# Kernel optimization log

Hardware: AMD Instinct MI355X
Metric: run time of the kernel (lower is better)

## Reference

```python
import jax, jax.numpy as jnp
import numpy as np

NUM_EXPERTS = 256
TOP_K = 8
N_GROUP = 8
TOPK_GROUP = 4
ROUTED_SCALING = 2.5
EXPERTS_PER_GROUP = NUM_EXPERTS // N_GROUP  # 32


def setup_inputs() -> dict:
    key = jax.random.key(0)
    k1, k2, k3 = jax.random.split(key, 3)
    hidden_states = jax.random.normal(k1, (8192, 7168), dtype=jnp.float32)
    weight = jax.random.normal(k2, (NUM_EXPERTS, 7168), dtype=jnp.float32) * 0.02
    e_score_correction_bias = jax.random.normal(k3, (NUM_EXPERTS,), dtype=jnp.float32) * 0.1
    return {
        "hidden_states": hidden_states,
        "weight": weight,
        "e_score_correction_bias": e_score_correction_bias,
    }


def reference(hidden_states, weight, e_score_correction_bias):
    # Router logits: [T, E]
    router_logits = jnp.einsum("th,eh->te", hidden_states, weight)
    scores = jax.nn.sigmoid(router_logits)
    scores_for_choice = scores + e_score_correction_bias  # [T, E]

    T = scores_for_choice.shape[0]
    # Group-limited selection (noaux_tc): group score = sum of top-2 experts in group
    grouped = scores_for_choice.reshape(T, N_GROUP, EXPERTS_PER_GROUP)
    group_top2, _ = jax.lax.top_k(grouped, 2)            # [T, G, 2]
    group_scores = group_top2.sum(axis=-1)               # [T, G]
    _, group_idx = jax.lax.top_k(group_scores, TOPK_GROUP)  # [T, topk_group]
    group_mask = jax.nn.one_hot(group_idx, N_GROUP, dtype=scores.dtype).max(axis=1)  # [T, G]
    expert_mask = jnp.repeat(group_mask, EXPERTS_PER_GROUP, axis=-1)  # [T, E]
    masked_scores = scores_for_choice * expert_mask

    # Final top-k experts; routing weights gathered from raw sigmoid scores
    _, selected_experts = jax.lax.top_k(masked_scores, TOP_K)         # [T, K] int32
    routing_weights = jnp.take_along_axis(scores, selected_experts, axis=-1)  # [T, K]
    routing_weights = routing_weights / (routing_weights.sum(axis=-1, keepdims=True) + 1e-20)
    routing_weights = routing_weights * ROUTED_SCALING
    return routing_weights, selected_experts
```

## Files before the change

### kernel.cpp

```cpp
#include <hip/hip_runtime.h>
#include <math.h>
#include <stdint.h>

#define T_TOK 8192
#define NEXP  256
#define HD    7168
#define PLANE ((size_t)T_TOK * NEXP)
#define SCALE 4096.0f
#define INV_S2 (1.0f / 16777216.0f)
#define BM 64
#define BK 32
#define NSTEP_TOT (HD / BK)
#define BIMG_STEP 32768

typedef _Float16 h8  __attribute__((ext_vector_type(8)));
typedef float f32x16 __attribute__((ext_vector_type(16)));
typedef __attribute__((address_space(3))) uint8_t       lds_t;
typedef __attribute__((address_space(1))) const uint8_t gbl_t;

__global__ __launch_bounds__(256) void wconv(const float* __restrict__ W,
                                             _Float16* __restrict__ img) {
  const int cc  = blockIdx.x * 256 + threadIdx.x;
  const int t   = cc >> 11;
  const int c   = cc & 2047;
  const int hl  = c >> 10;
  const int rem = c & 1023;
  const int row = rem >> 2;
  const int sp  = rem & 3;
  const int sl  = sp ^ ((row >> 1) & 3);
  const int k   = t * BK + sl * 8;

  const float* src = W + (size_t)row * HD + k;
  const float4 v0 = *(const float4*)src;
  const float4 v1 = *(const float4*)(src + 4);
  const float xs[8] = {v0.x, v0.y, v0.z, v0.w, v1.x, v1.y, v1.z, v1.w};
  h8 out;
#pragma unroll
  for (int j = 0; j < 8; ++j) {
    const float v = xs[j] * SCALE;
    const _Float16 hh = (_Float16)v;
    out[j] = hl ? (_Float16)(v - (float)hh) : hh;
  }
  *(h8*)(img + (size_t)cc * 8) = out;
}

__global__ __launch_bounds__(256, 2) void router_gemm(
    const float* __restrict__ X, const _Float16* __restrict__ img,
    float* __restrict__ partial, int S) {
  __shared__ __align__(1024) _Float16 As[2][2][BM][BK];
  __shared__ __align__(1024) _Float16 Bs[2][2][NEXP][BK];

  const int tid = threadIdx.x;
  const int id  = blockIdx.x;
  const int sb  = id % S;
  const int mb  = id / S;

  const int row0  = mb * BM;
  const int nstep = (HD / S) / BK;
  const int tbase = sb * nstep;

  const int lane = tid & 63, wv = tid >> 6;
  const int r31 = lane & 31, kg = lane >> 5;

  const int sm = tid >> 2;
  const int sk = tid & 3;
  const int spA = sk ^ ((sm >> 1) & 3);

  const float* Ap = X + (size_t)(row0 + sm) * HD + tbase * BK + sk * 8;
  const uint8_t* imgB = (const uint8_t*)img + (size_t)tbase * BIMG_STEP + tid * 16;

  f32x16 accP[2][2], accQ[2][2];
#pragma unroll
  for (int i = 0; i < 2; ++i)
#pragma unroll
    for (int j = 0; j < 2; ++j) { accP[i][j] = (f32x16)(0.f); accQ[i][j] = (f32x16)(0.f); }

#define STAGE_B(t, b)                                                          \
  {                                                                            \
    const uint8_t* g = imgB + (size_t)(t) * BIMG_STEP;                         \
    uint8_t* l = (uint8_t*)&Bs[b][0][0][0] + tid * 16;                         \
    _Pragma("unroll")                                                          \
    for (int i = 0; i < 8; ++i)                                                \
      __builtin_amdgcn_global_load_lds((gbl_t*)(uintptr_t)(g + i * 4096),      \
                                       (lds_t*)(uintptr_t)(l + i * 4096),      \
                                       16, 0, 0);                              \
  }

#define CVT_WRITE_A(b, va, vb)                                                 \
  {                                                                            \
    const float xs[8] = {va.x, va.y, va.z, va.w, vb.x, vb.y, vb.z, vb.w};      \
    h8 hv, lv_;                                                                \
    _Pragma("unroll")                                                          \
    for (int j = 0; j < 8; ++j) {                                              \
      const float v = xs[j] * SCALE;                                           \
      const _Float16 hh = (_Float16)v;                                         \
      hv[j] = hh; lv_[j] = (_Float16)(v - (float)hh);                          \
    }                                                                          \
    *(h8*)&As[b][0][sm][spA * 8] = hv;                                         \
    *(h8*)&As[b][1][sm][spA * 8] = lv_;                                        \
  }

  {
    const float4 a0 = *(const float4*)(Ap);
    const float4 a1 = *(const float4*)(Ap + 4);
    __builtin_amdgcn_sched_barrier(0);
    STAGE_B(0, 0);
    asm volatile("s_waitcnt vmcnt(0)" ::: "memory");
    __builtin_amdgcn_sched_barrier(0);
    CVT_WRITE_A(0, a0, a1);
    asm volatile("s_waitcnt lgkmcnt(0)" ::: "memory");
    __builtin_amdgcn_s_barrier();
  }

  for (int t = 0; t < nstep; ++t) {
    const int cur = t & 1;
    const int nxt = cur ^ 1;
    const bool more = (t + 1 < nstep);

    float4 a0, a1;
    if (more) {
      const float* ap = Ap + (size_t)(t + 1) * BK;
      a0 = *(const float4*)(ap);
      a1 = *(const float4*)(ap + 4);
      __builtin_amdgcn_sched_barrier(0);
      STAGE_B(t + 1, nxt);
      __builtin_amdgcn_sched_barrier(0);
    }

    h8 aH[2][2], aL[2][2], bH[2][2], bL[2][2];
#pragma unroll
    for (int ks = 0; ks < 2; ++ks) {
#pragma unroll
      for (int mi = 0; mi < 2; ++mi) {
        const int row = mi * 32 + r31;
        const int sp  = (ks * 2 + kg) ^ ((row >> 1) & 3);
        aH[ks][mi] = *(const h8*)&As[cur][0][row][sp * 8];
        aL[ks][mi] = *(const h8*)&As[cur][1][row][sp * 8];
      }
#pragma unroll
      for (int ni = 0; ni < 2; ++ni) {
        const int col = wv * 64 + ni * 32 + r31;
        const int sp  = (ks * 2 + kg) ^ ((col >> 1) & 3);
        bH[ks][ni] = *(const h8*)&Bs[cur][0][col][sp * 8];
        bL[ks][ni] = *(const h8*)&Bs[cur][1][col][sp * 8];
      }
      __builtin_amdgcn_sched_barrier(0);
    }

    asm volatile("s_waitcnt lgkmcnt(8)" ::: "memory");
    __builtin_amdgcn_sched_barrier(0);
    __builtin_amdgcn_s_setprio(1);
#pragma unroll
    for (int mi = 0; mi < 2; ++mi)
#pragma unroll
      for (int ni = 0; ni < 2; ++ni)
        accP[mi][ni] = __builtin_amdgcn_mfma_f32_32x32x16_f16(aH[0][mi], bH[0][ni], accP[mi][ni], 0, 0, 0);
#pragma unroll
    for (int mi = 0; mi < 2; ++mi)
#pragma unroll
      for (int ni = 0; ni < 2; ++ni)
        accQ[mi][ni] = __builtin_amdgcn_mfma_f32_32x32x16_f16(aL[0][mi], bH[0][ni], accQ[mi][ni], 0, 0, 0);
#pragma unroll
    for (int mi = 0; mi < 2; ++mi)
#pragma unroll
      for (int ni = 0; ni < 2; ++ni)
        accQ[mi][ni] = __builtin_amdgcn_mfma_f32_32x32x16_f16(aH[0][mi], bL[0][ni], accQ[mi][ni], 0, 0, 0);

    asm volatile("s_waitcnt lgkmcnt(0)" ::: "memory");
    __builtin_amdgcn_sched_barrier(0);
#pragma unroll
    for (int mi = 0; mi < 2; ++mi)
#pragma unroll
      for (int ni = 0; ni < 2; ++ni)
        accP[mi][ni] = __builtin_amdgcn_mfma_f32_32x32x16_f16(aH[1][mi], bH[1][ni], accP[mi][ni], 0, 0, 0);
#pragma unroll
    for (int mi = 0; mi < 2; ++mi)
#pragma unroll
      for (int ni = 0; ni < 2; ++ni)
        accQ[mi][ni] = __builtin_amdgcn_mfma_f32_32x32x16_f16(aL[1][mi], bH[1][ni], accQ[mi][ni], 0, 0, 0);
#pragma unroll
    for (int mi = 0; mi < 2; ++mi)
#pragma unroll
      for (int ni = 0; ni < 2; ++ni)
        accQ[mi][ni] = __builtin_amdgcn_mfma_f32_32x32x16_f16(aH[1][mi], bL[1][ni], accQ[mi][ni], 0, 0, 0);
    __builtin_amdgcn_s_setprio(0);

    if (more) {
      asm volatile("s_waitcnt vmcnt(8)" ::: "memory");
      __builtin_amdgcn_sched_barrier(0);
      CVT_WRITE_A(nxt, a0, a1);
      asm volatile("s_waitcnt vmcnt(0) lgkmcnt(0)" ::: "memory");
      __builtin_amdgcn_s_barrier();
    }
  }

  float* base = partial + (size_t)sb * PLANE;
#pragma unroll
  for (int mi = 0; mi < 2; ++mi)
#pragma unroll
    for (int ni = 0; ni < 2; ++ni) {
      const f32x16 acc = accP[mi][ni] + accQ[mi][ni];
      const int col = wv * 64 + ni * 32 + r31;
#pragma unroll
      for (int reg = 0; reg < 16; ++reg) {
        const int rr  = (reg & 3) + 8 * (reg >> 2) + 4 * kg;
        const int row = row0 + mi * 32 + rr;
        base[(size_t)row * NEXP + col] = acc[reg];
      }
    }
}

__global__ __launch_bounds__(256) void gate_kernel(const float* __restrict__ logits,
                                                   const float* __restrict__ bias,
                                                   float* __restrict__ out_w,
                                                   float* __restrict__ out_e, int S) {
    const int wave = threadIdx.x >> 6;
    const int lane = threadIdx.x & 63;
    const int t = blockIdx.x * 4 + wave;
    if (t >= T_TOK) return;

    float l4[4] = {0.f, 0.f, 0.f, 0.f};
    for (int s = 0; s < S; ++s) {
        const float4 v = *(const float4*)(&logits[(size_t)s * PLANE + (size_t)t * NEXP + lane * 4]);
        l4[0] += v.x; l4[1] += v.y; l4[2] += v.z; l4[3] += v.w;
    }
    const float4 bv = *(const float4*)(&bias[lane * 4]);

    float s4[4], c[4];
#pragma unroll
    for (int j = 0; j < 4; ++j) s4[j] = 1.f / (1.f + expf(-l4[j] * INV_S2));
    c[0] = s4[0] + bv.x;
    c[1] = s4[1] + bv.y;
    c[2] = s4[2] + bv.z;
    c[3] = s4[3] + bv.w;

    float a = fmaxf(c[0], c[1]), b = fminf(c[0], c[1]);
    float d = fmaxf(c[2], c[3]), e = fminf(c[2], c[3]);
    float m1 = fmaxf(a, d);
    float m2 = fmaxf(fminf(a, d), fmaxf(b, e));
#pragma unroll
    for (int off = 1; off < 8; off <<= 1) {
        const float o1 = __shfl_xor(m1, off);
        const float o2 = __shfl_xor(m2, off);
        const float n1 = fmaxf(m1, o1);
        const float n2 = fmaxf(fminf(m1, o1), fmaxf(m2, o2));
        m1 = n1; m2 = n2;
    }
    const float gs = m1 + m2;
    const int   g  = lane >> 3;

    int rank = 0;
#pragma unroll
    for (int gg = 0; gg < 8; ++gg) {
        const float og = __shfl(gs, gg * 8);
        rank += (og > gs) || (og == gs && gg < g);
    }
    const bool gsel = rank < 4;

    float v[4];
#pragma unroll
    for (int j = 0; j < 4; ++j) v[j] = gsel ? c[j] : 0.0f;

    float selw = 0.f;
    int   seli = 0;
    float wsum = 0.f;

#pragma unroll
    for (int k = 0; k < 8; ++k) {
        float bvv = v[0]; int bi = lane * 4; float br = s4[0];
#pragma unroll
        for (int j = 1; j < 4; ++j) {
            if (v[j] > bvv) { bvv = v[j]; bi = lane * 4 + j; br = s4[j]; }
        }
#pragma unroll
        for (int off = 32; off > 0; off >>= 1) {
            const float ov = __shfl_xor(bvv, off);
            const int   oi = __shfl_xor(bi, off);
            const float orr = __shfl_xor(br, off);
            if (ov > bvv || (ov == bvv && oi < bi)) { bvv = ov; bi = oi; br = orr; }
        }
        if (lane == k) { selw = br; seli = bi; }
        wsum += br;
        const int rem = bi - lane * 4;
#pragma unroll
        for (int j = 0; j < 4; ++j)
            if (rem == j) v[j] = -INFINITY;
    }

    if (lane < 8) {
        const float w = selw / (wsum + 1e-20f) * 2.5f;
        out_w[(size_t)t * 8 + lane] = w;
        out_e[(size_t)t * 8 + lane] = (float)seli;
    }
}

extern "C" void kernel_launch(void* const* d_in, const int* in_sizes, int n_in,
                              void* d_out, int out_size, void* d_ws, size_t ws_size,
                              hipStream_t stream) {
    const float* X    = (const float*)d_in[0];
    const float* W    = (const float*)d_in[1];
    const float* bias = (const float*)d_in[2];
    float* out = (float*)d_out;

    _Float16* img = (_Float16*)d_ws;
    const size_t woff = (size_t)NSTEP_TOT * BIMG_STEP;
    float* partial = (float*)((char*)d_ws + woff);

    int S = 1;
    if (ws_size >= woff + 4 * PLANE * sizeof(float)) S = 4;
    else if (ws_size >= woff + 2 * PLANE * sizeof(float)) S = 2;

    wconv<<<dim3(NSTEP_TOT * 2048 / 256), 256, 0, stream>>>(W, img);
    router_gemm<<<dim3((T_TOK / BM) * S), 256, 0, stream>>>(X, img, partial, S);
    gate_kernel<<<dim3(T_TOK / 4), 256, 0, stream>>>(partial, bias, out, out + (size_t)T_TOK * 8, S);
}
```

Baseline: 143.5 us.

## Load B fragments directly from global in MFMA layout, drop LDS staging

The weight image is reorganised so each lane can read its MFMA B-operand fragments straight from global memory, which removes the B tile from shared memory and the global_load_lds staging. The two accumulator sets are merged into one, and the hand-placed waitcnt, sched_barrier and setprio scheduling is replaced by a plain __syncthreads at the top of each step. This cuts LDS traffic and register pressure and may allow higher occupancy, but B loads are now issued from global in the same step they are consumed with no prefetch, so load latency is exposed. Multiple waves also re-read the same B data through cache.

Result: slower. 147.1 us (+2.5%).

```diff
diff --git a/kernel.cpp b/kernel.cpp
--- a/kernel.cpp
+++ b/kernel.cpp
@@ -11,26 +11,23 @@
 #define BM 64
 #define BK 32
 #define NSTEP_TOT (HD / BK)
-#define BIMG_STEP 32768
+#define IMG_STEP_H 16384
 
 typedef _Float16 h8  __attribute__((ext_vector_type(8)));
 typedef float f32x16 __attribute__((ext_vector_type(16)));
-typedef __attribute__((address_space(3))) uint8_t       lds_t;
-typedef __attribute__((address_space(1))) const uint8_t gbl_t;
 
 __global__ __launch_bounds__(256) void wconv(const float* __restrict__ W,
                                              _Float16* __restrict__ img) {
   const int cc  = blockIdx.x * 256 + threadIdx.x;
   const int t   = cc >> 11;
   const int c   = cc & 2047;
-  const int hl  = c >> 10;
-  const int rem = c & 1023;
-  const int row = rem >> 2;
-  const int sp  = rem & 3;
-  const int sl  = sp ^ ((row >> 1) & 3);
-  const int k   = t * BK + sl * 8;
-
-  const float* src = W + (size_t)row * HD + k;
+  const int ks  = c >> 10;
+  const int pl  = (c >> 9) & 1;
+  const int col = (c >> 1) & 255;
+  const int kg  = c & 1;
+  const int k   = t * BK + ks * 16 + kg * 8;
+
+  const float* src = W + (size_t)col * HD + k;
   const float4 v0 = *(const float4*)src;
   const float4 v1 = *(const float4*)(src + 4);
   const float xs[8] = {v0.x, v0.y, v0.z, v0.w, v1.x, v1.y, v1.z, v1.w};
@@ -39,16 +36,15 @@
   for (int j = 0; j < 8; ++j) {
     const float v = xs[j] * SCALE;
     const _Float16 hh = (_Float16)v;
-    out[j] = hl ? (_Float16)(v - (float)hh) : hh;
+    out[j] = pl ? (_Float16)(v - (float)hh) : hh;
   }
   *(h8*)(img + (size_t)cc * 8) = out;
 }
 
-__global__ __launch_bounds__(256, 2) void router_gemm(
+__global__ __launch_bounds__(256) void router_gemm(
     const float* __restrict__ X, const _Float16* __restrict__ img,
     float* __restrict__ partial, int S) {
-  __shared__ __align__(1024) _Float16 As[2][2][BM][BK];
-  __shared__ __align__(1024) _Float16 Bs[2][2][NEXP][BK];
+  __shared__ _Float16 As[2][2][BM][BK];
 
   const int tid = threadIdx.x;
   const int id  = blockIdx.x;
@@ -67,24 +63,15 @@
   const int spA = sk ^ ((sm >> 1) & 3);
 
   const float* Ap = X + (size_t)(row0 + sm) * HD + tbase * BK + sk * 8;
-  const uint8_t* imgB = (const uint8_t*)img + (size_t)tbase * BIMG_STEP + tid * 16;
-
-  f32x16 accP[2][2], accQ[2][2];
+
+  const _Float16* imgBase = img + (size_t)tbase * IMG_STEP_H;
+  const int colb = wv * 64 + r31;
+
+  f32x16 acc[2][2];
 #pragma unroll
   for (int i = 0; i < 2; ++i)
 #pragma unroll
-    for (int j = 0; j < 2; ++j) { accP[i][j] = (f32x16)(0.f); accQ[i][j] = (f32x16)(0.f); }
-
-#define STAGE_B(t, b)                                                          \
-  {                                                                            \
-    const uint8_t* g = imgB + (size_t)(t) * BIMG_STEP;                         \
-    uint8_t* l = (uint8_t*)&Bs[b][0][0][0] + tid * 16;                         \
-    _Pragma("unroll")                                                          \
-    for (int i = 0; i < 8; ++i)                                                \
-      __builtin_amdgcn_global_load_lds((gbl_t*)(uintptr_t)(g + i * 4096),      \
-                                       (lds_t*)(uintptr_t)(l + i * 4096),      \
-                                       16, 0, 0);                              \
-  }
+    for (int j = 0; j < 2; ++j) acc[i][j] = (f32x16)(0.f);
 
 #define CVT_WRITE_A(b, va, vb)                                                 \
   {                                                                            \
@@ -103,33 +90,34 @@
   {
     const float4 a0 = *(const float4*)(Ap);
     const float4 a1 = *(const float4*)(Ap + 4);
-    __builtin_amdgcn_sched_barrier(0);
-    STAGE_B(0, 0);
-    asm volatile("s_waitcnt vmcnt(0)" ::: "memory");
-    __builtin_amdgcn_sched_barrier(0);
     CVT_WRITE_A(0, a0, a1);
-    asm volatile("s_waitcnt lgkmcnt(0)" ::: "memory");
-    __builtin_amdgcn_s_barrier();
   }
 
   for (int t = 0; t < nstep; ++t) {
     const int cur = t & 1;
-    const int nxt = cur ^ 1;
     const bool more = (t + 1 < nstep);
+    __syncthreads();
+
+    const _Float16* bp = imgBase + (size_t)t * IMG_STEP_H;
+    h8 b[2][2][2];
+#pragma unroll
+    for (int ks = 0; ks < 2; ++ks)
+#pragma unroll
+      for (int pl = 0; pl < 2; ++pl)
+#pragma unroll
+        for (int ni = 0; ni < 2; ++ni)
+          b[ks][pl][ni] = *(const h8*)(bp + ((size_t)((ks * 2 + pl) * 256 + colb + ni * 32) * 16) + kg * 8);
 
     float4 a0, a1;
     if (more) {
       const float* ap = Ap + (size_t)(t + 1) * BK;
       a0 = *(const float4*)(ap);
       a1 = *(const float4*)(ap + 4);
-      __builtin_amdgcn_sched_barrier(0);
-      STAGE_B(t + 1, nxt);
-      __builtin_amdgcn_sched_barrier(0);
-    }
-
-    h8 aH[2][2], aL[2][2], bH[2][2], bL[2][2];
-#pragma unroll
-    for (int ks = 0; ks < 2; ++ks) {
+    }
+
+    h8 aH[2][2], aL[2][2];
+#pragma unroll
+    for (int ks = 0; ks < 2; ++ks)
 #pragma unroll
       for (int mi = 0; mi < 2; ++mi) {
         const int row = mi * 32 + r31;
@@ -137,60 +125,28 @@
         aH[ks][mi] = *(const h8*)&As[cur][0][row][sp * 8];
         aL[ks][mi] = *(const h8*)&As[cur][1][row][sp * 8];
       }
-#pragma unroll
-      for (int ni = 0; ni < 2; ++ni) {
-        const int col = wv * 64 + ni * 32 + r31;
-        const int sp  = (ks * 2 + kg) ^ ((col >> 1) & 3);
-        bH[ks][ni] = *(const h8*)&Bs[cur][0][col][sp * 8];
-        bL[ks][ni] = *(const h8*)&Bs[cur][1][col][sp * 8];
-      }
-      __builtin_amdgcn_sched_barrier(0);
-    }
-
-    asm volatile("s_waitcnt lgkmcnt(8)" ::: "memory");
-    __builtin_amdgcn_sched_barrier(0);
-    __builtin_amdgcn_s_setprio(1);
-#pragma unroll
-    for (int mi = 0; mi < 2; ++mi)
-#pragma unroll
-      for (int ni = 0; ni < 2; ++ni)
-        accP[mi][ni] = __builtin_amdgcn_mfma_f32_32x32x16_f16(aH[0][mi], bH[0][ni], accP[mi][ni], 0, 0, 0);
-#pragma unroll
-    for (int mi = 0; mi < 2; ++mi)
-#pragma unroll
-      for (int ni = 0; ni < 2; ++ni)
-        accQ[mi][ni] = __builtin_amdgcn_mfma_f32_32x32x16_f16(aL[0][mi], bH[0][ni], accQ[mi][ni], 0, 0, 0);
-#pragma unroll
-    for (int mi = 0; mi < 2; ++mi)
-#pragma unroll
-      for (int ni = 0; ni < 2; ++ni)
-        accQ[mi][ni] = __builtin_amdgcn_mfma_f32_32x32x16_f16(aH[0][mi], bL[0][ni], accQ[mi][ni], 0, 0, 0);
-
-    asm volatile("s_waitcnt lgkmcnt(0)" ::: "memory");
-    __builtin_amdgcn_sched_barrier(0);
-#pragma unroll
-    for (int mi = 0; mi < 2; ++mi)
-#pragma unroll
-      for (int ni = 0; ni < 2; ++ni)
-        accP[mi][ni] = __builtin_amdgcn_mfma_f32_32x32x16_f16(aH[1][mi], bH[1][ni], accP[mi][ni], 0, 0, 0);
-#pragma unroll
-    for (int mi = 0; mi < 2; ++mi)
-#pragma unroll
-      for (int ni = 0; ni < 2; ++ni)
-        accQ[mi][ni] = __builtin_amdgcn_mfma_f32_32x32x16_f16(aL[1][mi], bH[1][ni], accQ[mi][ni], 0, 0, 0);
-#pragma unroll
-    for (int mi = 0; mi < 2; ++mi)
-#pragma unroll
-      for (int ni = 0; ni < 2; ++ni)
-        accQ[mi][ni] = __builtin_amdgcn_mfma_f32_32x32x16_f16(aH[1][mi], bL[1][ni], accQ[mi][ni], 0, 0, 0);
-    __builtin_amdgcn_s_setprio(0);
+
+#pragma unroll
+    for (int ks = 0; ks < 2; ++ks) {
+#pragma unroll
+      for (int mi = 0; mi < 2; ++mi)
+#pragma unroll
+        for (int ni = 0; ni < 2; ++ni)
+          acc[mi][ni] = __builtin_amdgcn_mfma_f32_32x32x16_f16(aH[ks][mi], b[ks][0][ni], acc[mi][ni], 0, 0, 0);
+#pragma unroll
+      for (int mi = 0; mi < 2; ++mi)
+#pragma unroll
+        for (int ni = 0; ni < 2; ++ni)
+          acc[mi][ni] = __builtin_amdgcn_mfma_f32_32x32x16_f16(aL[ks][mi], b[ks][0][ni], acc[mi][ni], 0, 0, 0);
+#pragma unroll
+      for (int mi = 0; mi < 2; ++mi)
+#pragma unroll
+        for (int ni = 0; ni < 2; ++ni)
+          acc[mi][ni] = __builtin_amdgcn_mfma_f32_32x32x16_f16(aH[ks][mi], b[ks][1][ni], acc[mi][ni], 0, 0, 0);
+    }
 
     if (more) {
-      asm volatile("s_waitcnt vmcnt(8)" ::: "memory");
-      __builtin_amdgcn_sched_barrier(0);
-      CVT_WRITE_A(nxt, a0, a1);
-      asm volatile("s_waitcnt vmcnt(0) lgkmcnt(0)" ::: "memory");
-      __builtin_amdgcn_s_barrier();
+      CVT_WRITE_A(cur ^ 1, a0, a1);
     }
   }
 
@@ -199,13 +155,12 @@
   for (int mi = 0; mi < 2; ++mi)
 #pragma unroll
     for (int ni = 0; ni < 2; ++ni) {
-      const f32x16 acc = accP[mi][ni] + accQ[mi][ni];
       const int col = wv * 64 + ni * 32 + r31;
 #pragma unroll
       for (int reg = 0; reg < 16; ++reg) {
         const int rr  = (reg & 3) + 8 * (reg >> 2) + 4 * kg;
         const int row = row0 + mi * 32 + rr;
-        base[(size_t)row * NEXP + col] = acc[reg];
+        base[(size_t)row * NEXP + col] = acc[mi][ni][reg];
       }
     }
 }
@@ -303,7 +258,7 @@
     float* out = (float*)d_out;
 
     _Float16* img = (_Float16*)d_ws;
-    const size_t woff = (size_t)NSTEP_TOT * BIMG_STEP;
+    const size_t woff = (size_t)NSTEP_TOT * IMG_STEP_H * sizeof(_Float16);
     float* partial = (float*)((char*)d_ws + woff);
 
     int S = 1;
```
